# Kernel optimization log

Measured on AMD Instinct MI355X. Metric: run time of the kernel, lower is better.

The kernel has to match this reference:

```python
import jax, jax.numpy as jnp
import numpy as np

D_MODEL = 256
N_HEAD = 8
D_FF = 2048
B, N = 8, 1024
NEG = -9e15
EPS = 1e-5


def _layernorm(x, g, b):
    mu = jnp.mean(x, axis=-1, keepdims=True)
    var = jnp.mean(jnp.square(x - mu), axis=-1, keepdims=True)
    return (x - mu) * jax.lax.rsqrt(var + EPS) * g + b


def setup_inputs() -> dict:
    key = jax.random.key(0)
    ks = jax.random.split(key, 12)
    d, dff = D_MODEL, D_FF
    s = 1.0 / np.sqrt(d)
    inp = {
        "src": jax.random.normal(ks[0], (B, N, d), dtype=jnp.float32),
        "adj": jax.random.randint(ks[1], (B, N, N), 0, 2, dtype=jnp.int32),
        "W_gat": jax.random.normal(ks[2], (d, d), dtype=jnp.float32) * s,
        "a_gat": jax.random.normal(ks[3], (2 * d, 1), dtype=jnp.float32) * s,
        "in_proj_w": jax.random.normal(ks[4], (3 * d, d), dtype=jnp.float32) * s,
        "in_proj_b": jnp.zeros((3 * d,), dtype=jnp.float32),
        "out_proj_w": jax.random.normal(ks[5], (d, d), dtype=jnp.float32) * s,
        "out_proj_b": jnp.zeros((d,), dtype=jnp.float32),
        "lin1_w": jax.random.normal(ks[6], (dff, d), dtype=jnp.float32) * s,
        "lin1_b": jnp.zeros((dff,), dtype=jnp.float32),
        "lin2_w": jax.random.normal(ks[7], (d, dff), dtype=jnp.float32) * (1.0 / np.sqrt(dff)),
        "lin2_b": jnp.zeros((d,), dtype=jnp.float32),
        "ln1_g": jnp.ones((d,), dtype=jnp.float32),
        "ln1_b": jnp.zeros((d,), dtype=jnp.float32),
        "ln2_g": jnp.ones((d,), dtype=jnp.float32),
        "ln2_b": jnp.zeros((d,), dtype=jnp.float32),
        "ln3_g": jnp.ones((d,), dtype=jnp.float32),
        "ln3_b": jnp.zeros((d,), dtype=jnp.float32),
    }
    return inp


def reference(src, adj, W_gat, a_gat, in_proj_w, in_proj_b, out_proj_w, out_proj_b,
              lin1_w, lin1_b, lin2_w, lin2_b, ln1_g, ln1_b, ln2_g, ln2_b, ln3_g, ln3_b):
    d = D_MODEL
    # --- Graph attention (dropout inactive in eval) ---
    Wh = jnp.matmul(src, W_gat)                      # [B,N,d]
    a1 = a_gat[:d, 0]
    a2 = a_gat[d:, 0]
    # e[b,i,j] = Wh_i . a1 + Wh_j . a2  (equivalent to concat+matmul in source)
    f1 = Wh @ a1                                     # [B,N]
    f2 = Wh @ a2                                     # [B,N]
    e = f1[:, :, None] + f2[:, None, :]              # [B,N,N]
    e = jnp.where(adj > 0, e, NEG)
    attn = jax.nn.softmax(e, axis=-1)
    h_prime = jnp.matmul(attn, Wh)                   # [B,N,d]
    graph_out = jax.nn.elu(h_prime)
    x = _layernorm(src + graph_out, ln1_g, ln1_b)

    # --- Multi-head self-attention ---
    qkv = x @ in_proj_w.T + in_proj_b                # [B,N,3d]
    q, k, v = jnp.split(qkv, 3, axis=-1)
    hd = d // N_HEAD
    def heads(t):
        return t.reshape(B, N, N_HEAD, hd).transpose(0, 2, 1, 3)  # [B,H,N,hd]
    q, k, v = heads(q), heads(k), heads(v)
    scores = jnp.einsum("bhid,bhjd->bhij", q, k) / np.sqrt(hd)
    probs = jax.nn.softmax(scores, axis=-1)
    ctx = jnp.einsum("bhij,bhjd->bhid", probs, v)
    ctx = ctx.transpose(0, 2, 1, 3).reshape(B, N, d)
    attn_out = ctx @ out_proj_w.T + out_proj_b
    y = _layernorm(x + attn_out, ln2_g, ln2_b)

    # --- FFN ---
    ff = jax.nn.relu(y @ lin1_w.T + lin1_b) @ lin2_w.T + lin2_b
    return _layernorm(y + ff, ln3_g, ln3_b)
```

## Files before the change

kernel.cpp:

```cpp
#include <hip/hip_runtime.h>
#include <math.h>

constexpr int BATCH = 8;
constexpr int SEQ   = 1024;
constexpr int DM    = 256;
constexpr int DF    = 2048;
constexpr int NH    = 8;
constexpr int HDIM  = 32;
constexpr int ROWS  = BATCH * SEQ;
constexpr float NEGV = -9e15f;
constexpr float EPSV = 1e-5f;
constexpr float QSCALE = 0.2550351822f;
constexpr float LOG2E  = 1.44269504f;

typedef __attribute__((ext_vector_type(8))) short short8;
typedef __attribute__((ext_vector_type(4))) float f32x4;

static __device__ __forceinline__ ushort f2bf(float f) {
    unsigned x = __float_as_uint(f);
    unsigned r = (x + 0x7fffu + ((x >> 16) & 1u)) >> 16;
    return (ushort)r;
}
static __device__ __forceinline__ unsigned cvt_pk_bf16(float lo, float hi) {
    unsigned r;
    asm volatile("v_cvt_pk_bf16_f32 %0, %1, %2" : "=v"(r) : "v"(lo), "v"(hi));
    return r;
}

struct CastArgs {
    const float* in[5];
    ushort* out[5];
    int n4[5];
};
constexpr int CAST_BLKS = (2097152 + 196608 + 65536 + 524288 + 524288) / 4 / 256;

__global__ __launch_bounds__(256) void prep_k(CastArgs a,
                                              const float* __restrict__ W_gat,
                                              const float* __restrict__ a_gat,
                                              ushort* __restrict__ wgTb,
                                              float* __restrict__ w1,
                                              float* __restrict__ w2)
{
    __shared__ float Ts[32][33];
    const int bid = blockIdx.x;
    const int t = threadIdx.x;

    if (bid < CAST_BLKS) {
        int idx = bid * 256 + t;
        #pragma unroll
        for (int r = 0; r < 5; r++) {
            if (idx < a.n4[r]) {
                float4 v = *(const float4*)&a.in[r][(size_t)idx * 4];
                ushort4 o; o.x = f2bf(v.x); o.y = f2bf(v.y); o.z = f2bf(v.z); o.w = f2bf(v.w);
                *(ushort4*)&a.out[r][(size_t)idx * 4] = o;
                return;
            }
            idx -= a.n4[r];
        }
    } else if (bid < CAST_BLKS + 64) {
        const int bb = bid - CAST_BLKS;
        const int r0 = (bb >> 3) * 32, c0 = (bb & 7) * 32;
        const int lr = t >> 3, lc4 = (t & 7) * 4;
        float4 v = *(const float4*)&W_gat[(size_t)(r0 + lr) * DM + c0 + lc4];
        Ts[lr][lc4] = v.x; Ts[lr][lc4 + 1] = v.y; Ts[lr][lc4 + 2] = v.z; Ts[lr][lc4 + 3] = v.w;
        __syncthreads();
        const int oc = t >> 3, or4 = (t & 7) * 4;
        ushort4 o;
        o.x = f2bf(Ts[or4 + 0][oc]); o.y = f2bf(Ts[or4 + 1][oc]);
        o.z = f2bf(Ts[or4 + 2][oc]); o.w = f2bf(Ts[or4 + 3][oc]);
        *(ushort4*)&wgTb[(size_t)(c0 + oc) * DM + r0 + or4] = o;
    } else {
        const int k = (bid - CAST_BLKS - 64) * 4 + (t >> 6);
        const int l = t & 63;
        float4 wv = *(const float4*)&W_gat[(size_t)k * DM + 4 * l];
        float4 a1 = *(const float4*)&a_gat[4 * l];
        float4 a2 = *(const float4*)&a_gat[DM + 4 * l];
        float s1 = wv.x*a1.x + wv.y*a1.y + wv.z*a1.z + wv.w*a1.w;
        float s2 = wv.x*a2.x + wv.y*a2.y + wv.z*a2.z + wv.w*a2.w;
        #pragma unroll
        for (int off = 32; off; off >>= 1) {
            s1 += __shfl_xor(s1, off, 64);
            s2 += __shfl_xor(s2, off, 64);
        }
        if (l == 0) { w1[k] = s1; w2[k] = s2; }
    }
}

__global__ __launch_bounds__(256) void f12_k(const float* __restrict__ src,
                                             const float* __restrict__ w1,
                                             const float* __restrict__ w2,
                                             float* __restrict__ f1,
                                             float* __restrict__ f2)
{
    const int t = threadIdx.x;
    const size_t row = (size_t)blockIdx.x * 4 + (t >> 6);
    const int l = t & 63;
    float s1 = 0.f, s2 = 0.f;
    #pragma unroll
    for (int i = 0; i < 4; i++) {
        float v = src[row * DM + l + 64*i];
        s1 = fmaf(v, w1[l + 64*i], s1);
        s2 = fmaf(v, w2[l + 64*i], s2);
    }
    #pragma unroll
    for (int off = 32; off; off >>= 1) {
        s1 += __shfl_xor(s1, off, 64);
        s2 += __shfl_xor(s2, off, 64);
    }
    if (l == 0) { f1[row] = s1 * LOG2E; f2[row] = s2 * LOG2E; }
}

template<int EP, int BM, int BN>
__global__ __launch_bounds__(256) void gemm_bf(const ushort* __restrict__ A,
                                               const ushort* __restrict__ B,
                                               const float* __restrict__ bias,
                                               float* __restrict__ Cf,
                                               ushort* __restrict__ Cb,
                                               int N, int K, int ldB,
                                               long long sA, long long sB, long long sC)
{
    __shared__ ushort As[2][BM][40];
    __shared__ ushort Bs[2][BN][40];
    A += (size_t)blockIdx.z * sA;
    B += (size_t)blockIdx.z * sB;

    const int t  = threadIdx.x;
    const int m0 = blockIdx.y * BM, n0 = blockIdx.x * BN;
    const int lane = t & 63, lo = lane & 15, hi = lane >> 4;
    const int w = t >> 6;
    constexpr int NI = BM / 32, NJ = BN / 32;
    const int wr = (w >> 1) * (BM / 2);
    const int wc = (w & 1) * (BN / 2);

    const int lrA = (BM == 128) ? (t >> 1) : (t >> 2);
    const int lcA = (BM == 128) ? ((t & 1) * 16) : ((t & 3) * 8);
    const int lrB = (BN == 128) ? (t >> 1) : (t >> 2);
    const int lcB = (BN == 128) ? ((t & 1) * 16) : ((t & 3) * 8);

    f32x4 acc[NI][NJ];
    const f32x4 zero = {0.f, 0.f, 0.f, 0.f};
    #pragma unroll
    for (int i = 0; i < NI; i++)
        #pragma unroll
        for (int j = 0; j < NJ; j++) acc[i][j] = zero;

    const ushort* Ap = A + (size_t)(m0 + lrA) * K + lcA;
    const ushort* Bp = B + (size_t)(n0 + lrB) * ldB + lcB;

    short8 ar0, ar1, br0, br1;
    ar0 = *(const short8*)(Ap);
    if constexpr (BM == 128) ar1 = *(const short8*)(Ap + 8);
    br0 = *(const short8*)(Bp);
    if constexpr (BN == 128) br1 = *(const short8*)(Bp + 8);
    *(short8*)&As[0][lrA][lcA] = ar0;
    if constexpr (BM == 128) *(short8*)&As[0][lrA][lcA + 8] = ar1;
    *(short8*)&Bs[0][lrB][lcB] = br0;
    if constexpr (BN == 128) *(short8*)&Bs[0][lrB][lcB + 8] = br1;

    const int NT = K >> 5;
    for (int it = 0; it < NT; it++) {
        const int cur = it & 1;
        if (it + 1 < NT) {
            const int k0 = (it + 1) << 5;
            ar0 = *(const short8*)(Ap + k0);
            if constexpr (BM == 128) ar1 = *(const short8*)(Ap + k0 + 8);
            br0 = *(const short8*)(Bp + k0);
            if constexpr (BN == 128) br1 = *(const short8*)(Bp + k0 + 8);
        }
        __syncthreads();

        short8 afr[NI], bfr[NJ];
        #pragma unroll
        for (int i = 0; i < NI; i++) afr[i] = *(const short8*)&As[cur][wr + i*16 + lo][hi * 8];
        #pragma unroll
        for (int j = 0; j < NJ; j++) bfr[j] = *(const short8*)&Bs[cur][wc + j*16 + lo][hi * 8];
        #pragma unroll
        for (int i = 0; i < NI; i++)
            #pragma unroll
            for (int j = 0; j < NJ; j++)
                acc[i][j] = __builtin_amdgcn_mfma_f32_16x16x32_bf16(afr[i], bfr[j], acc[i][j], 0, 0, 0);

        if (it + 1 < NT) {
            *(short8*)&As[cur ^ 1][lrA][lcA] = ar0;
            if constexpr (BM == 128) *(short8*)&As[cur ^ 1][lrA][lcA + 8] = ar1;
            *(short8*)&Bs[cur ^ 1][lrB][lcB] = br0;
            if constexpr (BN == 128) *(short8*)&Bs[cur ^ 1][lrB][lcB + 8] = br1;
        }
    }

    if (EP == 2 || EP == 5 || EP == 6) Cb += (size_t)blockIdx.z * sC;
    else                               Cf += (size_t)blockIdx.z * sC;
    #pragma unroll
    for (int j = 0; j < NJ; j++) {
        const int col = n0 + wc + j * 16 + lo;
        float bj = (EP == 1 || EP == 2 || EP == 6) ? bias[col] : 0.f;
        #pragma unroll
        for (int i = 0; i < NI; i++) {
            const int rbase = m0 + wr + i * 16 + hi * 4;
            #pragma unroll
            for (int r = 0; r < 4; r++) {
                float v = acc[i][j][r] + bj;
                if (EP == 3) v = v > 0.f ? v : expm1f(v);
                if (EP == 2) v = fmaxf(v, 0.f);
                if (EP == 6 && col < DM) v *= QSCALE;
                if (EP == 2 || EP == 5 || EP == 6) Cb[(size_t)(rbase + r) * N + col] = f2bf(v);
                else                               Cf[(size_t)(rbase + r) * N + col] = v;
            }
        }
    }
}

template<bool WB>
__global__ __launch_bounds__(256) void ln_k(const float* __restrict__ a,
                                            const float* __restrict__ r,
                                            const float* __restrict__ g,
                                            const float* __restrict__ be,
                                            float* __restrict__ o,
                                            ushort* __restrict__ ob)
{
    const size_t row = (size_t)blockIdx.x * 4 + (threadIdx.x >> 6);
    const int l = threadIdx.x & 63;
    const float* pa = a + row * DM;
    const float* pr = r + row * DM;
    float v[4]; float s = 0.f;
    #pragma unroll
    for (int i = 0; i < 4; i++) { v[i] = pa[l + 64*i] + pr[l + 64*i]; s += v[i]; }
    #pragma unroll
    for (int off = 32; off; off >>= 1) s += __shfl_xor(s, off, 64);
    float mu = s * (1.0f / DM);
    float q = 0.f;
    #pragma unroll
    for (int i = 0; i < 4; i++) { float d = v[i] - mu; q += d * d; }
    #pragma unroll
    for (int off = 32; off; off >>= 1) q += __shfl_xor(q, off, 64);
    float rs = rsqrtf(q * (1.0f / DM) + EPSV);
    #pragma unroll
    for (int i = 0; i < 4; i++) {
        int c = l + 64*i;
        float out = (v[i] - mu) * rs * g[c] + be[c];
        o[row * DM + c] = out;
        if (WB) ob[row * DM + c] = f2bf(out);
    }
}

__global__ __launch_bounds__(256) void gat_sm_k(const int* __restrict__ adj,
                                                const float* __restrict__ f1,
                                                const float* __restrict__ f2,
                                                ushort* __restrict__ P)
{
    __shared__ float red[8];
    const int i = blockIdx.x, b = i >> 10;
    const int t = threadIdx.x;
    const int4 a4 = *(const int4*)&adj[(size_t)i * SEQ + 4 * t];
    const float4 f4 = *(const float4*)&f2[(size_t)(b << 10) + 4 * t];
    const float f1i = f1[i];
    float e[4];
    e[0] = a4.x > 0 ? f1i + f4.x : NEGV;
    e[1] = a4.y > 0 ? f1i + f4.y : NEGV;
    e[2] = a4.z > 0 ? f1i + f4.z : NEGV;
    e[3] = a4.w > 0 ? f1i + f4.w : NEGV;
    float mx = fmaxf(fmaxf(e[0], e[1]), fmaxf(e[2], e[3]));
    #pragma unroll
    for (int off = 32; off; off >>= 1) mx = fmaxf(mx, __shfl_xor(mx, off, 64));
    if ((t & 63) == 0) red[t >> 6] = mx;
    __syncthreads();
    mx = fmaxf(fmaxf(red[0], red[1]), fmaxf(red[2], red[3]));
    float s = 0.f;
    #pragma unroll
    for (int u = 0; u < 4; u++) { e[u] = exp2f(e[u] - mx); s += e[u]; }
    #pragma unroll
    for (int off = 32; off; off >>= 1) s += __shfl_xor(s, off, 64);
    if ((t & 63) == 0) red[4 + (t >> 6)] = s;
    __syncthreads();
    float inv = 1.0f / (red[4] + red[5] + red[6] + red[7]);
    ushort4 o;
    o.x = f2bf(e[0] * inv); o.y = f2bf(e[1] * inv);
    o.z = f2bf(e[2] * inv); o.w = f2bf(e[3] * inv);
    *(ushort4*)&P[(size_t)i * SEQ + 4 * t] = o;
}

__device__ __forceinline__ int vt_idx(int d, int kv) { return d * 72 + ((d >> 3) & 3) * 16 + kv; }
constexpr int VTSZ = 32 * 72 + 3 * 16 + 8;

__global__ __launch_bounds__(256) void mha_k(const ushort* __restrict__ qkv,
                                             ushort* __restrict__ ctxb)
{
    __shared__ ushort Ks[2][64][40];
    __shared__ ushort Vt[2][VTSZ];
    __shared__ ushort Ps[64][72];

    const int blk = blockIdx.x;
    const int qt = blk & 15, h = (blk >> 4) & 7, b = blk >> 7;
    const int i0 = qt << 6;
    const int t = threadIdx.x;
    const int w = t >> 6, lane = t & 63, lo = lane & 15, hi = lane >> 4;
    const int gsh = lane & 48;
    const size_t base = (size_t)b * SEQ * 768;

    const short8 aQ = *(const short8*)(qkv + base + (size_t)(i0 + 16*w + lo) * 768 + h * HDIM + hi * 8);
    short8 ones;
    #pragma unroll
    for (int e = 0; e < 8; e++) ones[e] = (short)0x3F80;

    const int srow = t >> 2, scb = (t & 3) << 3;
    const int vcol = (srow & 32) | ((srow & 15) << 1) | ((srow >> 4) & 1);
    {
        const ushort* p0 = qkv + base + (size_t)srow * 768 + h * HDIM;
        short8 k0 = *(const short8*)(p0 + 256 + scb);
        short8 v0 = *(const short8*)(p0 + 512 + scb);
        *(short8*)&Ks[0][srow][scb] = k0;
        #pragma unroll
        for (int e = 0; e < 8; e++) Vt[0][vt_idx(scb + e, vcol)] = (ushort)v0[e];
    }

    float m_run[4], l_run[4];
    f32x4 O0 = {0.f, 0.f, 0.f, 0.f}, O1 = {0.f, 0.f, 0.f, 0.f};
    #pragma unroll
    for (int r = 0; r < 4; r++) { m_run[r] = -3.0e38f; l_run[r] = 0.f; }
    const f32x4 zero = {0.f, 0.f, 0.f, 0.f};

    short8 kreg, vreg;
    for (int it = 0; it < 16; it++) {
        const int cur = it & 1;
        if (it < 15) {
            const ushort* nb = qkv + base + (size_t)((it + 1) * 64 + srow) * 768 + h * HDIM;
            kreg = *(const short8*)(nb + 256 + scb);
            vreg = *(const short8*)(nb + 512 + scb);
        }
        __syncthreads();

        f32x4 S[4];
        #pragma unroll
        for (int jt = 0; jt < 4; jt++) {
            short8 bK = *(const short8*)&Ks[cur][16 * jt + lo][hi * 8];
            S[jt] = __builtin_amdgcn_mfma_f32_16x16x32_bf16(aQ, bK, zero, 0, 0, 0);
        }

        float mxl[4];
        bool any = false;
        #pragma unroll
        for (int r = 0; r < 4; r++) {
            mxl[r] = fmaxf(fmaxf(S[0][r], S[1][r]), fmaxf(S[2][r], S[3][r]));
            any = any || (mxl[r] > m_run[r] + 8.f);
        }
        unsigned long long bal = __ballot(any);
        if ((bal >> gsh) & 0xffffULL) {
            #pragma unroll
            for (int r = 0; r < 4; r++) {
                float mx = mxl[r];
                #pragma unroll
                for (int off = 8; off; off >>= 1) mx = fmaxf(mx, __shfl_xor(mx, off, 16));
                float mnew = fmaxf(m_run[r], mx);
                float sc = exp2f(m_run[r] - mnew);
                m_run[r] = mnew;
                l_run[r] *= sc; O0[r] *= sc; O1[r] *= sc;
            }
        }
        #pragma unroll
        for (int r = 0; r < 4; r++) {
            const int row = 16 * w + 4 * hi + r;
            unsigned u01 = cvt_pk_bf16(exp2f(S[0][r] - m_run[r]), exp2f(S[1][r] - m_run[r]));
            unsigned u23 = cvt_pk_bf16(exp2f(S[2][r] - m_run[r]), exp2f(S[3][r] - m_run[r]));
            *(unsigned*)&Ps[row][2 * lo]      = u01;
            *(unsigned*)&Ps[row][32 + 2 * lo] = u23;
        }

        f32x4 O2 = zero;
        #pragma unroll
        for (int kt = 0; kt < 2; kt++) {
            short8 aP  = *(const short8*)&Ps[16 * w + lo][32 * kt + hi * 8];
            short8 bV0 = *(const short8*)&Vt[cur][vt_idx(lo,      32 * kt + hi * 8)];
            short8 bV1 = *(const short8*)&Vt[cur][vt_idx(16 + lo, 32 * kt + hi * 8)];
            O0 = __builtin_amdgcn_mfma_f32_16x16x32_bf16(aP, bV0, O0, 0, 0, 0);
            O1 = __builtin_amdgcn_mfma_f32_16x16x32_bf16(aP, bV1, O1, 0, 0, 0);
            O2 = __builtin_amdgcn_mfma_f32_16x16x32_bf16(aP, ones, O2, 0, 0, 0);
        }
        #pragma unroll
        for (int r = 0; r < 4; r++) l_run[r] += O2[r];

        if (it < 15) {
            *(short8*)&Ks[cur ^ 1][srow][scb] = kreg;
            #pragma unroll
            for (int e = 0; e < 8; e++) Vt[cur ^ 1][vt_idx(scb + e, vcol)] = (ushort)vreg[e];
        }
    }

    #pragma unroll
    for (int r = 0; r < 4; r++) {
        float inv = 1.0f / l_run[r];
        size_t row = (size_t)b * SEQ + i0 + 16 * w + 4 * hi + r;
        ctxb[row * DM + h * HDIM + lo]      = f2bf(O0[r] * inv);
        ctxb[row * DM + h * HDIM + 16 + lo] = f2bf(O1[r] * inv);
    }
}

extern "C" void kernel_launch(void* const* d_in, const int* in_sizes, int n_in,
                              void* d_out, int out_size, void* d_ws, size_t ws_size,
                              hipStream_t stream)
{
    const float* src        = (const float*)d_in[0];
    const int*   adj        = (const int*)  d_in[1];
    const float* W_gat      = (const float*)d_in[2];
    const float* a_gat      = (const float*)d_in[3];
    const float* in_proj_w  = (const float*)d_in[4];
    const float* in_proj_b  = (const float*)d_in[5];
    const float* out_proj_w = (const float*)d_in[6];
    const float* out_proj_b = (const float*)d_in[7];
    const float* lin1_w     = (const float*)d_in[8];
    const float* lin1_b     = (const float*)d_in[9];
    const float* lin2_w     = (const float*)d_in[10];
    const float* lin2_b     = (const float*)d_in[11];
    const float* ln1_g      = (const float*)d_in[12];
    const float* ln1_b_     = (const float*)d_in[13];
    const float* ln2_g      = (const float*)d_in[14];
    const float* ln2_b_     = (const float*)d_in[15];
    const float* ln3_g      = (const float*)d_in[16];
    const float* ln3_b_     = (const float*)d_in[17];

    char* base = (char*)d_ws;
    const size_t MB = 1024 * 1024;
    float*  tmp   = (float*) (base + 0 * MB);
    float*  x     = (float*) (base + 8 * MB);
    float*  y     = (float*) (base + 16 * MB);
    ushort* P_bf  = (ushort*)(base + 24 * MB);
    ushort* qkvb  = (ushort*)(base + 24 * MB);
    ushort* ff1b  = (ushort*)(base + 24 * MB);
    ushort* srcb  = (ushort*)(base + 56 * MB);
    ushort* WhTb  = (ushort*)(base + 60 * MB);
    ushort* xb    = (ushort*)(base + 64 * MB);
    ushort* yb    = (ushort*)(base + 68 * MB);
    ushort* ctxb  = (ushort*)(base + 72 * MB);
    float*  f1    = (float*) (base + 76 * MB);
    float*  f2    = f1 + ROWS;
    float*  w1    = f2 + ROWS;
    float*  w2    = w1 + DM;
    ushort* wgTb  = (ushort*)(base + 77 * MB);
    ushort* ipwb  = wgTb + 65536;
    ushort* opwb  = ipwb + 196608;
    ushort* l1wb  = opwb + 65536;
    ushort* l2wb  = l1wb + 524288;

    dim3 b256(256);

    CastArgs ca;
    ca.in[0] = src;       ca.out[0] = srcb; ca.n4[0] = 2097152 / 4;
    ca.in[1] = in_proj_w; ca.out[1] = ipwb; ca.n4[1] = 196608 / 4;
    ca.in[2] = out_proj_w;ca.out[2] = opwb; ca.n4[2] = 65536 / 4;
    ca.in[3] = lin1_w;    ca.out[3] = l1wb; ca.n4[3] = 524288 / 4;
    ca.in[4] = lin2_w;    ca.out[4] = l2wb; ca.n4[4] = 524288 / 4;
    prep_k<<<CAST_BLKS + 64 + 64, b256, 0, stream>>>(ca, W_gat, a_gat, wgTb, w1, w2);

    f12_k<<<ROWS / 4, b256, 0, stream>>>(src, w1, w2, f1, f2);
    gemm_bf<5, 64, 64><<<dim3(ROWS/64, DM/64, 1), b256, 0, stream>>>(wgTb, srcb, nullptr, nullptr, WhTb,
                                                                     ROWS, DM, DM, 0, 0, 0);
    gat_sm_k<<<ROWS, b256, 0, stream>>>(adj, f1, f2, P_bf);
    gemm_bf<3, 64, 64><<<dim3(DM/64, SEQ/64, 8), b256, 0, stream>>>(P_bf, WhTb, nullptr, tmp, nullptr,
                                                                    DM, SEQ, ROWS,
                                                                    (long long)SEQ * SEQ, (long long)SEQ, (long long)SEQ * DM);
    ln_k<true><<<ROWS / 4, b256, 0, stream>>>(src, tmp, ln1_g, ln1_b_, x, xb);

    gemm_bf<6, 128, 64><<<dim3(768/64, ROWS/128, 1), b256, 0, stream>>>(xb, ipwb, in_proj_b, nullptr, qkvb,
                                                                        768, DM, DM, 0, 0, 0);
    mha_k<<<BATCH * NH * (SEQ / 64), b256, 0, stream>>>(qkvb, ctxb);
    gemm_bf<1, 64, 64><<<dim3(DM/64, ROWS/64, 1), b256, 0, stream>>>(ctxb, opwb, out_proj_b, tmp, nullptr,
                                                                     DM, DM, DM, 0, 0, 0);
    ln_k<true><<<ROWS / 4, b256, 0, stream>>>(x, tmp, ln2_g, ln2_b_, y, yb);

    gemm_bf<2, 128, 128><<<dim3(DF/128, ROWS/128, 1), b256, 0, stream>>>(yb, l1wb, lin1_b, nullptr, ff1b,
                                                                         DF, DM, DM, 0, 0, 0);
    gemm_bf<1, 64, 64><<<dim3(DM/64, ROWS/64, 1), b256, 0, stream>>>(ff1b, l2wb, lin2_b, tmp, nullptr,
                                                                     DM, DF, DF, 0, 0, 0);
    ln_k<false><<<ROWS / 4, b256, 0, stream>>>(y, tmp, ln3_g, ln3_b_, (float*)d_out, nullptr);
}
```

Measured before the change: 163.8 us.

## Store GEMM residual outputs as bf16, vectorize LN and f12, wave-per-row GAT softmax

All GEMM epilogues now write bf16 into a single temp buffer, so the residual tensors read by layernorm are half the size. The layernorm and f12 kernels use float4 loads and stores. The GAT softmax processes one row per wavefront with no shared-memory reductions or block barriers. The MHA block index is remapped so that q-tiles vary slowest. Rounding the residual branches to bf16 before layernorm adds precision loss.

```diff
diff --git a/kernel.cpp b/kernel.cpp
--- a/kernel.cpp
+++ b/kernel.cpp
@@ -20,6 +20,9 @@
     unsigned x = __float_as_uint(f);
     unsigned r = (x + 0x7fffu + ((x >> 16) & 1u)) >> 16;
     return (ushort)r;
+}
+static __device__ __forceinline__ float bf2f(ushort u) {
+    return __uint_as_float((unsigned)u << 16);
 }
 static __device__ __forceinline__ unsigned cvt_pk_bf16(float lo, float hi) {
     unsigned r;
@@ -92,16 +95,13 @@
                                              float* __restrict__ f1,
                                              float* __restrict__ f2)
 {
-    const int t = threadIdx.x;
-    const size_t row = (size_t)blockIdx.x * 4 + (t >> 6);
-    const int l = t & 63;
-    float s1 = 0.f, s2 = 0.f;
-    #pragma unroll
-    for (int i = 0; i < 4; i++) {
-        float v = src[row * DM + l + 64*i];
-        s1 = fmaf(v, w1[l + 64*i], s1);
-        s2 = fmaf(v, w2[l + 64*i], s2);
-    }
+    const size_t row = (size_t)blockIdx.x * 4 + (threadIdx.x >> 6);
+    const int l = threadIdx.x & 63;
+    float4 sv = *(const float4*)&src[row * DM + 4 * l];
+    float4 v1 = *(const float4*)&w1[4 * l];
+    float4 v2 = *(const float4*)&w2[4 * l];
+    float s1 = sv.x*v1.x + sv.y*v1.y + sv.z*v1.z + sv.w*v1.w;
+    float s2 = sv.x*v2.x + sv.y*v2.y + sv.z*v2.z + sv.w*v2.w;
     #pragma unroll
     for (int off = 32; off; off >>= 1) {
         s1 += __shfl_xor(s1, off, 64);
@@ -114,7 +114,6 @@
 __global__ __launch_bounds__(256) void gemm_bf(const ushort* __restrict__ A,
                                                const ushort* __restrict__ B,
                                                const float* __restrict__ bias,
-                                               float* __restrict__ Cf,
                                                ushort* __restrict__ Cb,
                                                int N, int K, int ldB,
                                                long long sA, long long sB, long long sC)
@@ -188,8 +187,7 @@
         }
     }
 
-    if (EP == 2 || EP == 5 || EP == 6) Cb += (size_t)blockIdx.z * sC;
-    else                               Cf += (size_t)blockIdx.z * sC;
+    Cb += (size_t)blockIdx.z * sC;
     #pragma unroll
     for (int j = 0; j < NJ; j++) {
         const int col = n0 + wc + j * 16 + lo;
@@ -203,8 +201,7 @@
                 if (EP == 3) v = v > 0.f ? v : expm1f(v);
                 if (EP == 2) v = fmaxf(v, 0.f);
                 if (EP == 6 && col < DM) v *= QSCALE;
-                if (EP == 2 || EP == 5 || EP == 6) Cb[(size_t)(rbase + r) * N + col] = f2bf(v);
-                else                               Cf[(size_t)(rbase + r) * N + col] = v;
+                Cb[(size_t)(rbase + r) * N + col] = f2bf(v);
             }
         }
     }
@@ -212,7 +209,7 @@
 
 template<bool WB>
 __global__ __launch_bounds__(256) void ln_k(const float* __restrict__ a,
-                                            const float* __restrict__ r,
+                                            const ushort* __restrict__ r,
                                             const float* __restrict__ g,
                                             const float* __restrict__ be,
                                             float* __restrict__ o,
@@ -220,26 +217,32 @@
 {
     const size_t row = (size_t)blockIdx.x * 4 + (threadIdx.x >> 6);
     const int l = threadIdx.x & 63;
-    const float* pa = a + row * DM;
-    const float* pr = r + row * DM;
-    float v[4]; float s = 0.f;
-    #pragma unroll
-    for (int i = 0; i < 4; i++) { v[i] = pa[l + 64*i] + pr[l + 64*i]; s += v[i]; }
+    float4 av = *(const float4*)&a[row * DM + 4 * l];
+    ushort4 rv = *(const ushort4*)&r[row * DM + 4 * l];
+    float v0 = av.x + bf2f(rv.x);
+    float v1 = av.y + bf2f(rv.y);
+    float v2 = av.z + bf2f(rv.z);
+    float v3 = av.w + bf2f(rv.w);
+    float s = (v0 + v1) + (v2 + v3);
     #pragma unroll
     for (int off = 32; off; off >>= 1) s += __shfl_xor(s, off, 64);
-    float mu = s * (1.0f / DM);
-    float q = 0.f;
-    #pragma unroll
-    for (int i = 0; i < 4; i++) { float d = v[i] - mu; q += d * d; }
+    const float mu = s * (1.0f / DM);
+    float q = (v0-mu)*(v0-mu) + (v1-mu)*(v1-mu) + (v2-mu)*(v2-mu) + (v3-mu)*(v3-mu);
     #pragma unroll
     for (int off = 32; off; off >>= 1) q += __shfl_xor(q, off, 64);
-    float rs = rsqrtf(q * (1.0f / DM) + EPSV);
-    #pragma unroll
-    for (int i = 0; i < 4; i++) {
-        int c = l + 64*i;
-        float out = (v[i] - mu) * rs * g[c] + be[c];
-        o[row * DM + c] = out;
-        if (WB) ob[row * DM + c] = f2bf(out);
+    const float rs = rsqrtf(q * (1.0f / DM) + EPSV);
+    float4 gv = *(const float4*)&g[4 * l];
+    float4 bv = *(const float4*)&be[4 * l];
+    float4 ov;
+    ov.x = (v0 - mu) * rs * gv.x + bv.x;
+    ov.y = (v1 - mu) * rs * gv.y + bv.y;
+    ov.z = (v2 - mu) * rs * gv.z + bv.z;
+    ov.w = (v3 - mu) * rs * gv.w + bv.w;
+    *(float4*)&o[row * DM + 4 * l] = ov;
+    if (WB) {
+        ushort4 obv;
+        obv.x = f2bf(ov.x); obv.y = f2bf(ov.y); obv.z = f2bf(ov.z); obv.w = f2bf(ov.w);
+        *(ushort4*)&ob[row * DM + 4 * l] = obv;
     }
 }
 
@@ -248,35 +251,41 @@
                                                 const float* __restrict__ f2,
                                                 ushort* __restrict__ P)
 {
-    __shared__ float red[8];
-    const int i = blockIdx.x, b = i >> 10;
-    const int t = threadIdx.x;
-    const int4 a4 = *(const int4*)&adj[(size_t)i * SEQ + 4 * t];
-    const float4 f4 = *(const float4*)&f2[(size_t)(b << 10) + 4 * t];
-    const float f1i = f1[i];
-    float e[4];
-    e[0] = a4.x > 0 ? f1i + f4.x : NEGV;
-    e[1] = a4.y > 0 ? f1i + f4.y : NEGV;
-    e[2] = a4.z > 0 ? f1i + f4.z : NEGV;
-    e[3] = a4.w > 0 ? f1i + f4.w : NEGV;
-    float mx = fmaxf(fmaxf(e[0], e[1]), fmaxf(e[2], e[3]));
+    const int row = blockIdx.x * 4 + (threadIdx.x >> 6);
+    const int b = row >> 10;
+    const int l = threadIdx.x & 63;
+    const int* arow = adj + (size_t)row * SEQ;
+    const float* f2b = f2 + ((size_t)b << 10);
+    const float f1i = f1[row];
+
+    float e[16];
+    float mx = -3.4e38f;
+    #pragma unroll
+    for (int u = 0; u < 4; u++) {
+        const int j = 4 * l + 256 * u;
+        int4 a4 = *(const int4*)&arow[j];
+        float4 f4 = *(const float4*)&f2b[j];
+        e[4*u+0] = a4.x > 0 ? f1i + f4.x : NEGV;
+        e[4*u+1] = a4.y > 0 ? f1i + f4.y : NEGV;
+        e[4*u+2] = a4.z > 0 ? f1i + f4.z : NEGV;
+        e[4*u+3] = a4.w > 0 ? f1i + f4.w : NEGV;
+        mx = fmaxf(mx, fmaxf(fmaxf(e[4*u], e[4*u+1]), fmaxf(e[4*u+2], e[4*u+3])));
+    }
     #pragma unroll
     for (int off = 32; off; off >>= 1) mx = fmaxf(mx, __shfl_xor(mx, off, 64));
-    if ((t & 63) == 0) red[t >> 6] = mx;
-    __syncthreads();
-    mx = fmaxf(fmaxf(red[0], red[1]), fmaxf(red[2], red[3]));
     float s = 0.f;
     #pragma unroll
-    for (int u = 0; u < 4; u++) { e[u] = exp2f(e[u] - mx); s += e[u]; }
+    for (int k = 0; k < 16; k++) { e[k] = exp2f(e[k] - mx); s += e[k]; }
     #pragma unroll
     for (int off = 32; off; off >>= 1) s += __shfl_xor(s, off, 64);
-    if ((t & 63) == 0) red[4 + (t >> 6)] = s;
-    __syncthreads();
-    float inv = 1.0f / (red[4] + red[5] + red[6] + red[7]);
-    ushort4 o;
-    o.x = f2bf(e[0] * inv); o.y = f2bf(e[1] * inv);
-    o.z = f2bf(e[2] * inv); o.w = f2bf(e[3] * inv);
-    *(ushort4*)&P[(size_t)i * SEQ + 4 * t] = o;
+    const float inv = 1.0f / s;
+    #pragma unroll
+    for (int u = 0; u < 4; u++) {
+        ushort4 o;
+        o.x = f2bf(e[4*u+0] * inv); o.y = f2bf(e[4*u+1] * inv);
+        o.z = f2bf(e[4*u+2] * inv); o.w = f2bf(e[4*u+3] * inv);
+        *(ushort4*)&P[(size_t)row * SEQ + 4 * l + 256 * u] = o;
+    }
 }
 
 __device__ __forceinline__ int vt_idx(int d, int kv) { return d * 72 + ((d >> 3) & 3) * 16 + kv; }
@@ -290,7 +299,8 @@
     __shared__ ushort Ps[64][72];
 
     const int blk = blockIdx.x;
-    const int qt = blk & 15, h = (blk >> 4) & 7, b = blk >> 7;
+    const int grp = blk & 63, qt = blk >> 6;
+    const int h = grp & 7, b = grp >> 3;
     const int i0 = qt << 6;
     const int t = threadIdx.x;
     const int w = t >> 6, lane = t & 63, lo = lane & 15, hi = lane >> 4;
@@ -419,22 +429,22 @@
 
     char* base = (char*)d_ws;
     const size_t MB = 1024 * 1024;
-    float*  tmp   = (float*) (base + 0 * MB);
-    float*  x     = (float*) (base + 8 * MB);
-    float*  y     = (float*) (base + 16 * MB);
-    ushort* P_bf  = (ushort*)(base + 24 * MB);
-    ushort* qkvb  = (ushort*)(base + 24 * MB);
-    ushort* ff1b  = (ushort*)(base + 24 * MB);
-    ushort* srcb  = (ushort*)(base + 56 * MB);
-    ushort* WhTb  = (ushort*)(base + 60 * MB);
-    ushort* xb    = (ushort*)(base + 64 * MB);
-    ushort* yb    = (ushort*)(base + 68 * MB);
-    ushort* ctxb  = (ushort*)(base + 72 * MB);
-    float*  f1    = (float*) (base + 76 * MB);
+    ushort* tmpb  = (ushort*)(base + 0 * MB);
+    float*  x     = (float*) (base + 4 * MB);
+    float*  y     = (float*) (base + 12 * MB);
+    ushort* P_bf  = (ushort*)(base + 20 * MB);
+    ushort* qkvb  = (ushort*)(base + 20 * MB);
+    ushort* ff1b  = (ushort*)(base + 20 * MB);
+    ushort* srcb  = (ushort*)(base + 52 * MB);
+    ushort* WhTb  = (ushort*)(base + 56 * MB);
+    ushort* xb    = (ushort*)(base + 60 * MB);
+    ushort* yb    = (ushort*)(base + 64 * MB);
+    ushort* ctxb  = (ushort*)(base + 68 * MB);
+    float*  f1    = (float*) (base + 72 * MB);
     float*  f2    = f1 + ROWS;
     float*  w1    = f2 + ROWS;
     float*  w2    = w1 + DM;
-    ushort* wgTb  = (ushort*)(base + 77 * MB);
+    ushort* wgTb  = (ushort*)(base + 73 * MB);
     ushort* ipwb  = wgTb + 65536;
     ushort* opwb  = ipwb + 196608;
     ushort* l1wb  = opwb + 65536;
@@ -451,24 +461,24 @@
     prep_k<<<CAST_BLKS + 64 + 64, b256, 0, stream>>>(ca, W_gat, a_gat, wgTb, w1, w2);
 
     f12_k<<<ROWS / 4, b256, 0, stream>>>(src, w1, w2, f1, f2);
-    gemm_bf<5, 64, 64><<<dim3(ROWS/64, DM/64, 1), b256, 0, stream>>>(wgTb, srcb, nullptr, nullptr, WhTb,
+    gemm_bf<5, 64, 64><<<dim3(ROWS/64, DM/64, 1), b256, 0, stream>>>(wgTb, srcb, nullptr, WhTb,
                                                                      ROWS, DM, DM, 0, 0, 0);
-    gat_sm_k<<<ROWS, b256, 0, stream>>>(adj, f1, f2, P_bf);
-    gemm_bf<3, 64, 64><<<dim3(DM/64, SEQ/64, 8), b256, 0, stream>>>(P_bf, WhTb, nullptr, tmp, nullptr,
+    gat_sm_k<<<ROWS / 4, b256, 0, stream>>>(adj, f1, f2, P_bf);
+    gemm_bf<3, 64, 64><<<dim3(DM/64, SEQ/64, 8), b256, 0, stream>>>(P_bf, WhTb, nullptr, tmpb,
                                                                     DM, SEQ, ROWS,
                                                                     (long long)SEQ * SEQ, (long long)SEQ, (long long)SEQ * DM);
-    ln_k<true><<<ROWS / 4, b256, 0, stream>>>(src, tmp, ln1_g, ln1_b_, x, xb);
-
-    gemm_bf<6, 128, 64><<<dim3(768/64, ROWS/128, 1), b256, 0, stream>>>(xb, ipwb, in_proj_b, nullptr, qkvb,
+    ln_k<true><<<ROWS / 4, b256, 0, stream>>>(src, tmpb, ln1_g, ln1_b_, x, xb);
+
+    gemm_bf<6, 128, 64><<<dim3(768/64, ROWS/128, 1), b256, 0, stream>>>(xb, ipwb, in_proj_b, qkvb,
                                                                         768, DM, DM, 0, 0, 0);
     mha_k<<<BATCH * NH * (SEQ / 64), b256, 0, stream>>>(qkvb, ctxb);
-    gemm_bf<1, 64, 64><<<dim3(DM/64, ROWS/64, 1), b256, 0, stream>>>(ctxb, opwb, out_proj_b, tmp, nullptr,
+    gemm_bf<1, 64, 64><<<dim3(DM/64, ROWS/64, 1), b256, 0, stream>>>(ctxb, opwb, out_proj_b, tmpb,
                                                                      DM, DM, DM, 0, 0, 0);
-    ln_k<true><<<ROWS / 4, b256, 0, stream>>>(x, tmp, ln2_g, ln2_b_, y, yb);
-
-    gemm_bf<2, 128, 128><<<dim3(DF/128, ROWS/128, 1), b256, 0, stream>>>(yb, l1wb, lin1_b, nullptr, ff1b,
+    ln_k<true><<<ROWS / 4, b256, 0, stream>>>(x, tmpb, ln2_g, ln2_b_, y, yb);
+
+    gemm_bf<2, 128, 128><<<dim3(DF/128, ROWS/128, 1), b256, 0, stream>>>(yb, l1wb, lin1_b, ff1b,
                                                                          DF, DM, DM, 0, 0, 0);
-    gemm_bf<1, 64, 64><<<dim3(DM/64, ROWS/64, 1), b256, 0, stream>>>(ff1b, l2wb, lin2_b, tmp, nullptr,
+    gemm_bf<1, 64, 64><<<dim3(DM/64, ROWS/64, 1), b256, 0, stream>>>(ff1b, l2wb, lin2_b, tmpb,
                                                                      DM, DF, DF, 0, 0, 0);
-    ln_k<false><<<ROWS / 4, b256, 0, stream>>>(y, tmp, ln3_g, ln3_b_, (float*)d_out, nullptr);
-}
+    ln_k<false><<<ROWS / 4, b256, 0, stream>>>(y, tmpb, ln3_g, ln3_b_, (float*)d_out, nullptr);
+}
```

After: 156.4 us. 4.5% less time.
